# Optimization experiments

Measured on AMD Instinct MI355X. Metric: run time of the kernel, lower is better.

The kernel has to match this reference:

```python
import jax, jax.numpy as jnp
import numpy as np

HIDDEN = 2560
NH = 32            # num_attention_heads
HD = HIDDEN // NH  # head_size = 80
RD = 32            # rotary_dim = int(0.4 * 80)
THETA = 10000.0
B, S = 2, 2048


def _rope_cos_sin(position_ids):
    # neox-style partial RoPE over the first RD dims of each head
    inv_freq = 1.0 / (THETA ** (jnp.arange(0, RD, 2, dtype=jnp.float32) / RD))  # [RD/2]
    freqs = position_ids.astype(jnp.float32)[..., None] * inv_freq  # [B,S,RD/2]
    return jnp.cos(freqs), jnp.sin(freqs)


def _apply_rope(x, cos, sin):
    # x: [B,S,NH,HD]; rotate first RD dims (neox: halves are paired)
    rot, rest = x[..., :RD], x[..., RD:]
    x1, x2 = rot[..., : RD // 2], rot[..., RD // 2:]
    c = cos[:, :, None, :]
    s = sin[:, :, None, :]
    o1 = x1 * c - x2 * s
    o2 = x2 * c + x1 * s
    return jnp.concatenate([o1, o2, rest], axis=-1)


def setup_inputs() -> dict:
    key = jax.random.key(0)
    ks = jax.random.split(key, 6)
    position_ids = jnp.tile(jnp.arange(S, dtype=jnp.int64)[None, :], (B, 1))
    return {
        "position_ids": position_ids,
        "hidden_states": jax.random.normal(ks[0], (B, S, HIDDEN), dtype=jnp.float32),
        "w_qkv": jax.random.normal(ks[1], (HIDDEN, 3 * HIDDEN), dtype=jnp.float32) * 0.02,
        "b_qkv": jax.random.normal(ks[2], (3 * HIDDEN,), dtype=jnp.float32) * 0.02,
        "w_dense": jax.random.normal(ks[3], (HIDDEN, HIDDEN), dtype=jnp.float32) * 0.02,
        "b_dense": jax.random.normal(ks[4], (HIDDEN,), dtype=jnp.float32) * 0.02,
    }


def reference(position_ids, hidden_states, w_qkv, b_qkv, w_dense, b_dense):
    scale = HD ** -0.5
    qkv = hidden_states @ w_qkv + b_qkv          # [B,S,3*HIDDEN]
    q, k, v = jnp.split(qkv, 3, axis=-1)
    q = q.reshape(B, S, NH, HD)
    k = k.reshape(B, S, NH, HD)
    v = v.reshape(B, S, NH, HD)
    cos, sin = _rope_cos_sin(position_ids)
    q = _apply_rope(q, cos, sin)
    k = _apply_rope(k, cos, sin)
    scores = jnp.einsum("bqhd,bkhd->bhqk", q, k) * scale  # [B,NH,S,S]
    causal = jnp.tril(jnp.ones((S, S), dtype=bool))
    scores = jnp.where(causal[None, None], scores, jnp.finfo(scores.dtype).min)
    probs = jax.nn.softmax(scores, axis=-1)
    attn = jnp.einsum("bhqk,bkhd->bqhd", probs, v).reshape(B, S, HIDDEN)
    return attn @ w_dense + b_dense
```

## Files before the change

### kernel.cpp

```cpp
#include <hip/hip_runtime.h>

#define S_LEN 2048
#define NHEAD 32
#define HD 80
#define DPAD 96
#define HIDDEN 2560
#define QKV_N 7680

typedef __attribute__((ext_vector_type(8))) short bf16x8;
typedef __attribute__((ext_vector_type(8))) unsigned short u16x8;
typedef __attribute__((ext_vector_type(4))) float f32x4;

__device__ __forceinline__ unsigned short f2bf(float f) {
  unsigned int u = __float_as_uint(f);
  u += 0x7fffu + ((u >> 16) & 1u);
  return (unsigned short)(u >> 16);
}
__device__ __forceinline__ float bf2f(unsigned short h) {
  return __uint_as_float(((unsigned int)h) << 16);
}

__device__ __forceinline__ void gload16(const void* g, void* l) {
  __builtin_amdgcn_global_load_lds((const __attribute__((address_space(1))) void*)g,
                                   (__attribute__((address_space(3))) void*)l, 16, 0, 0);
}

__global__ __launch_bounds__(256) void k_cvt(const float* __restrict__ in,
                                             unsigned short* __restrict__ out, int n4) {
  int i = blockIdx.x * 256 + threadIdx.x;
  if (i >= n4) return;
  float4 v = reinterpret_cast<const float4*>(in)[i];
  ushort4 o;
  o.x = f2bf(v.x); o.y = f2bf(v.y); o.z = f2bf(v.z); o.w = f2bf(v.w);
  reinterpret_cast<ushort4*>(out)[i] = o;
}

__global__ __launch_bounds__(256) void k_transpose_bf16(const float* __restrict__ in,
                                                        unsigned short* __restrict__ out,
                                                        int R, int C) {
  __shared__ float tile[64][65];
  int tc = blockIdx.x * 64, tr = blockIdx.y * 64;
  for (int i = threadIdx.x; i < 64 * 64; i += 256) {
    int r = i >> 6, c = i & 63;
    tile[r][c] = in[(size_t)(tr + r) * C + (tc + c)];
  }
  __syncthreads();
  for (int i = threadIdx.x; i < 64 * 64; i += 256) {
    int r = i >> 6, c = i & 63;
    out[(size_t)(tc + r) * R + (tr + c)] = f2bf(tile[c][r]);
  }
}

__global__ __launch_bounds__(512, 2) void k_gemm256(const unsigned short* __restrict__ A,
                                                    const unsigned short* __restrict__ Bt,
                                                    const float* __restrict__ bias,
                                                    unsigned short* __restrict__ Cbf,
                                                    float* __restrict__ Cf,
                                                    int M, int N, int K, int out_f32) {
  __shared__ unsigned short sA[4][8192];
  __shared__ unsigned short sB[4][8192];
  const int nbn = N >> 8;
  const int nwg = (M >> 8) * nbn;
  int wg = blockIdx.x;
  const int cpx = nwg >> 3;
  wg = (wg & 7) * cpx + (wg >> 3);
  const int bm = wg / nbn, bn = wg - bm * nbn;
  const int tid = threadIdx.x;
  const int lane = tid & 63, wave = tid >> 6;
  const int wr = wave >> 2, wc = wave & 3;
  const int lc = lane & 15, lr = lane >> 4;

  const int sub = (lane & 7) ^ (lane >> 3);
  const int rstage = wave * 16 + (lane >> 3) * 2 + (sub >> 2);
  const int cstage = (sub & 3) * 8;
  const unsigned short* Agp = A + (size_t)(bm * 256 + rstage) * K + cstage;
  const unsigned short* Bgp = Bt + (size_t)(bn * 256 + rstage) * K + cstage;
  const size_t halfoff = (size_t)128 * K;

  const int laneoff = ((lc >> 1) << 7) + ((((lc & 1) << 2) | lr) ^ (lc >> 1)) << 4 ? 0 : 0;
  const int loff = ((lc >> 1) << 7) + (((((lc & 1) << 2) | lr) ^ (lc >> 1)) << 4);
  (void)laneoff;

  f32x4 acc[8][4];
  const f32x4 zero = {0.f, 0.f, 0.f, 0.f};
#pragma unroll
  for (int m = 0; m < 8; ++m)
#pragma unroll
    for (int n = 0; n < 4; ++n) acc[m][n] = zero;

  const int NT = K >> 5;

#pragma unroll
  for (int t = 0; t < 3; ++t) {
    gload16(Agp + 0 * halfoff + t * 32, &sA[t][wave * 512]);
    gload16(Agp + 1 * halfoff + t * 32, &sA[t][4096 + wave * 512]);
    gload16(Bgp + 0 * halfoff + t * 32, &sB[t][wave * 512]);
    gload16(Bgp + 1 * halfoff + t * 32, &sB[t][4096 + wave * 512]);
  }

  const char* cA[4] = {(const char*)&sA[0][0], (const char*)&sA[1][0],
                       (const char*)&sA[2][0], (const char*)&sA[3][0]};
  const char* cB[4] = {(const char*)&sB[0][0], (const char*)&sB[1][0],
                       (const char*)&sB[2][0], (const char*)&sB[3][0]};

  const int nj = NT >> 2;
  for (int j = 0; j < nj; ++j) {
#pragma unroll
    for (int to = 0; to < 4; ++to) {
      const int t = (j << 2) + to;
      if (t < NT - 2)       asm volatile("s_waitcnt vmcnt(8)" ::: "memory");
      else if (t == NT - 2) asm volatile("s_waitcnt vmcnt(4)" ::: "memory");
      else                  asm volatile("s_waitcnt vmcnt(0)" ::: "memory");
      __builtin_amdgcn_s_barrier();
      asm volatile("" ::: "memory");
      const bool st = (t + 3) < NT;
      const int sb = (to + 3) & 3;
      const char* bufA = cA[to];
      const char* bufB = cB[to];

      bf16x8 af[4], bfr[4];
#pragma unroll
      for (int mi = 0; mi < 4; ++mi)
        af[mi] = *(const bf16x8*)(bufA + ((wr * 128 + mi * 16) << 6) + loff);
#pragma unroll
      for (int ni = 0; ni < 4; ++ni)
        bfr[ni] = *(const bf16x8*)(bufB + ((wc * 64 + ni * 16) << 6) + loff);
      if (st) {
        gload16(Agp + 0 * halfoff + (t + 3) * 32, &sA[sb][wave * 512]);
        gload16(Agp + 1 * halfoff + (t + 3) * 32, &sA[sb][4096 + wave * 512]);
      }
      __builtin_amdgcn_s_barrier();
      asm volatile("s_waitcnt lgkmcnt(0)" ::: "memory");
      __builtin_amdgcn_sched_barrier(0);
      __builtin_amdgcn_s_setprio(1);
#pragma unroll
      for (int mi = 0; mi < 4; ++mi)
#pragma unroll
        for (int ni = 0; ni < 4; ++ni)
          acc[mi][ni] = __builtin_amdgcn_mfma_f32_16x16x32_bf16(af[mi], bfr[ni], acc[mi][ni], 0, 0, 0);
      __builtin_amdgcn_s_setprio(0);
      __builtin_amdgcn_s_barrier();

      bf16x8 ag[4];
#pragma unroll
      for (int mi = 0; mi < 4; ++mi)
        ag[mi] = *(const bf16x8*)(bufA + ((wr * 128 + (mi + 4) * 16) << 6) + loff);
      if (st) {
        gload16(Bgp + 0 * halfoff + (t + 3) * 32, &sB[sb][wave * 512]);
        gload16(Bgp + 1 * halfoff + (t + 3) * 32, &sB[sb][4096 + wave * 512]);
      }
      __builtin_amdgcn_s_barrier();
      asm volatile("s_waitcnt lgkmcnt(0)" ::: "memory");
      __builtin_amdgcn_sched_barrier(0);
      __builtin_amdgcn_s_setprio(1);
#pragma unroll
      for (int mi = 0; mi < 4; ++mi)
#pragma unroll
        for (int ni = 0; ni < 4; ++ni)
          acc[mi + 4][ni] = __builtin_amdgcn_mfma_f32_16x16x32_bf16(ag[mi], bfr[ni], acc[mi + 4][ni], 0, 0, 0);
      __builtin_amdgcn_s_setprio(0);
    }
  }

  const int rowb = bm * 256 + wr * 128;
  const int colb = bn * 256 + wc * 64;
#pragma unroll
  for (int ni = 0; ni < 4; ++ni) {
    const int col = colb + ni * 16 + lc;
    const float bv = bias[col];
#pragma unroll
    for (int mf = 0; mf < 8; ++mf) {
#pragma unroll
      for (int jj = 0; jj < 4; ++jj) {
        const int row = rowb + mf * 16 + lr * 4 + jj;
        const float v = acc[mf][ni][jj] + bv;
        if (out_f32) Cf[(size_t)row * N + col] = v;
        else Cbf[(size_t)row * N + col] = f2bf(v);
      }
    }
  }
}

__global__ __launch_bounds__(256) void k_rope(const unsigned short* __restrict__ qkv,
                                              unsigned short* __restrict__ Qw,
                                              unsigned short* __restrict__ Kw,
                                              unsigned short* __restrict__ Vt) {
  const int blk = blockIdx.x;
  const int sc = blk & 31;
  const int bh = blk >> 5;
  const int b = bh >> 5, h = bh & 31;
  const int s0 = sc * 64;
  __shared__ float cs0[64][16], sn0[64][16];
  __shared__ unsigned short vbuf[64][82];
  const int tid = threadIdx.x;
  for (int i = tid; i < 64 * 16; i += 256) {
    int sl = i >> 4, fi = i & 15;
    float ang = (float)(s0 + sl) * __expf(-(float)fi * 0.575646273248511421f);
    cs0[sl][fi] = cosf(ang);
    sn0[sl][fi] = sinf(ang);
  }
  __syncthreads();
  const size_t row0 = (size_t)(b * S_LEN + s0) * QKV_N;
  const size_t obase = ((size_t)bh * S_LEN + s0) * DPAD;
  for (int i = tid; i < 64 * DPAD; i += 256) {
    int sl = i / DPAD, d = i - sl * DPAD;
    float qv = 0.f, kv = 0.f;
    if (d < HD) {
      const unsigned short* rp = qkv + row0 + (size_t)sl * QKV_N + h * HD;
      float q = bf2f(rp[d]), k = bf2f(rp[HIDDEN + d]);
      if (d < 16) {
        float c = cs0[sl][d], s = sn0[sl][d];
        float q2 = bf2f(rp[d + 16]), k2 = bf2f(rp[HIDDEN + d + 16]);
        qv = q * c - q2 * s;
        kv = k * c - k2 * s;
      } else if (d < 32) {
        float c = cs0[sl][d - 16], s = sn0[sl][d - 16];
        float q1 = bf2f(rp[d - 16]), k1 = bf2f(rp[HIDDEN + d - 16]);
        qv = q * c + q1 * s;
        kv = k * c + k1 * s;
      } else {
        qv = q; kv = k;
      }
    }
    Qw[obase + (size_t)sl * DPAD + d] = f2bf(qv * 0.111803398874989485f);
    Kw[obase + (size_t)sl * DPAD + d] = f2bf(kv);
  }
  for (int i = tid; i < 64 * HD; i += 256) {
    int sl = i / HD, d = i - sl * HD;
    vbuf[sl][d] = qkv[row0 + (size_t)sl * QKV_N + 2 * HIDDEN + h * HD + d];
  }
  __syncthreads();
  const size_t vtb = (size_t)bh * DPAD * S_LEN + s0;
  for (int i = tid; i < DPAD * 64; i += 256) {
    int d = i >> 6, sl = i & 63;
    Vt[vtb + (size_t)d * S_LEN + sl] = (d < HD) ? vbuf[sl][d] : (unsigned short)0;
  }
}

__global__ __launch_bounds__(256, 2) void k_attn(const unsigned short* __restrict__ Qw,
                                                 const unsigned short* __restrict__ Kw,
                                                 const unsigned short* __restrict__ Vt,
                                                 unsigned short* __restrict__ O) {
  __shared__ unsigned short sK[2][64 * 104];
  __shared__ unsigned short sV[2][80 * 72];
  __shared__ unsigned short sP[4][16 * 72];
  const int p = blockIdx.x;
  const int bh = blockIdx.y;
  const int b = bh >> 5, h = bh & 31;
  const int tid = threadIdx.x;
  const int wave = tid >> 6, lane = tid & 63;
  const int lr = lane >> 4, lc = lane & 15;
  unsigned short* Pw = &sP[wave][0];

  const unsigned short* Kh = Kw + (size_t)bh * S_LEN * DPAD;
  const unsigned short* Vh = Vt + (size_t)bh * DPAD * S_LEN;
  const unsigned short* Qh = Qw + (size_t)bh * S_LEN * DPAD;

  const int kr = tid >> 2, kc = (tid & 3) * 24;
  const int vr = tid >> 3, vc = (tid & 7) * 8;

  u16x8 kst0, kst1, kst2, vst0, vst1, vst2;
  auto gload = [&](int t) {
    const unsigned short* Kg = Kh + ((size_t)(t * 64 + kr)) * DPAD + kc;
    kst0 = *(const u16x8*)(Kg);
    kst1 = *(const u16x8*)(Kg + 8);
    kst2 = *(const u16x8*)(Kg + 16);
    const unsigned short* Vg = Vh + (size_t)vr * S_LEN + t * 64 + vc;
    vst0 = *(const u16x8*)(Vg);
    vst1 = *(const u16x8*)(Vg + 32 * S_LEN);
    if (tid < 128) vst2 = *(const u16x8*)(Vg + (size_t)64 * S_LEN);
  };
  auto swrite = [&](int buf) {
    *(u16x8*)&sK[buf][kr * 104 + kc] = kst0;
    *(u16x8*)&sK[buf][kr * 104 + kc + 8] = kst1;
    *(u16x8*)&sK[buf][kr * 104 + kc + 16] = kst2;
    *(u16x8*)&sV[buf][vr * 72 + vc] = vst0;
    *(u16x8*)&sV[buf][(vr + 32) * 72 + vc] = vst1;
    if (tid < 128) *(u16x8*)&sV[buf][(vr + 64) * 72 + vc] = vst2;
  };

  const f32x4 zero = {0.f, 0.f, 0.f, 0.f};

#pragma unroll 1
  for (int qi = 0; qi < 2; ++qi) {
    const int qt = qi ? (15 - p) : p;
    const int nt = 2 * qt + 2;
    const int wbase = qt * 128 + wave * 32;

    bf16x8 qf[2][3];
#pragma unroll
    for (int m = 0; m < 2; ++m)
#pragma unroll
      for (int ks = 0; ks < 3; ++ks)
        qf[m][ks] = *(const bf16x8*)&Qh[(size_t)(wbase + m * 16 + lc) * DPAD + ks * 32 + lr * 8];

    f32x4 oacc[2][5];
#pragma unroll
    for (int m = 0; m < 2; ++m)
#pragma unroll
      for (int n = 0; n < 5; ++n) oacc[m][n] = zero;
    float mrun[2] = {-1e30f, -1e30f}, lrun[2] = {0.f, 0.f};

    gload(0);
    __syncthreads();
    swrite(0);
    int cur = 0;

#pragma unroll 1
    for (int t = 0; t < nt; ++t) {
      __syncthreads();
      if (t + 1 < nt) gload(t + 1);
      const int ktb = t * 64;
      const bool act0 = ktb <= wbase + 15;
      const bool act1 = ktb <= wbase + 31;
      if (act1) {
        const unsigned short* Kc = sK[cur];
        const unsigned short* Vc = sV[cur];
        f32x4 sf[2][4];
#pragma unroll
        for (int n = 0; n < 4; ++n) {
          sf[0][n] = zero; sf[1][n] = zero;
#pragma unroll
          for (int ks = 0; ks < 3; ++ks) {
            bf16x8 kf = *(const bf16x8*)&Kc[(n * 16 + lc) * 104 + ks * 32 + lr * 8];
            if (act0) sf[0][n] = __builtin_amdgcn_mfma_f32_16x16x32_bf16(kf, qf[0][ks], sf[0][n], 0, 0, 0);
            sf[1][n] = __builtin_amdgcn_mfma_f32_16x16x32_bf16(kf, qf[1][ks], sf[1][n], 0, 0, 0);
          }
        }
        bf16x8 vf[5][2];
#pragma unroll
        for (int n = 0; n < 5; ++n)
#pragma unroll
          for (int ks = 0; ks < 2; ++ks)
            vf[n][ks] = *(const bf16x8*)&Vc[(n * 16 + lc) * 72 + ks * 32 + lr * 8];
#pragma unroll
        for (int m = 0; m < 2; ++m) {
          if (m == 0 && !act0) continue;
          const int qrow0 = wbase + m * 16;
          if (ktb + 63 > qrow0) {
#pragma unroll
            for (int n = 0; n < 4; ++n)
#pragma unroll
              for (int j = 0; j < 4; ++j)
                if (ktb + n * 16 + lr * 4 + j > qrow0 + lc) sf[m][n][j] = -1e30f;
          }
          float t0 = sf[m][0][0];
#pragma unroll
          for (int n = 0; n < 4; ++n)
#pragma unroll
            for (int j = 0; j < 4; ++j) t0 = fmaxf(t0, sf[m][n][j]);
          t0 = fmaxf(t0, __shfl_xor(t0, 16));
          t0 = fmaxf(t0, __shfl_xor(t0, 32));
          const float nm = fmaxf(mrun[m], t0);
          const float corrq = __expf(mrun[m] - nm);
          mrun[m] = nm;
          float ps = 0.f;
#pragma unroll
          for (int n = 0; n < 4; ++n)
#pragma unroll
            for (int j = 0; j < 4; ++j) {
              float e = __expf(sf[m][n][j] - nm);
              sf[m][n][j] = e;
              ps += e;
            }
          ps += __shfl_xor(ps, 16);
          ps += __shfl_xor(ps, 32);
          lrun[m] = lrun[m] * corrq + ps;
          float cj[4];
#pragma unroll
          for (int j = 0; j < 4; ++j) cj[j] = __shfl(corrq, lr * 4 + j, 16);
#pragma unroll
          for (int n = 0; n < 5; ++n)
#pragma unroll
            for (int j = 0; j < 4; ++j) oacc[m][n][j] *= cj[j];
#pragma unroll
          for (int n = 0; n < 4; ++n) {
            unsigned lo = (unsigned)f2bf(sf[m][n][0]) | ((unsigned)f2bf(sf[m][n][1]) << 16);
            unsigned hi = (unsigned)f2bf(sf[m][n][2]) | ((unsigned)f2bf(sf[m][n][3]) << 16);
            uint2 u; u.x = lo; u.y = hi;
            *(uint2*)&Pw[lc * 72 + n * 16 + lr * 4] = u;
          }
          asm volatile("" ::: "memory");
          bf16x8 pa0 = *(const bf16x8*)&Pw[lc * 72 + lr * 8];
          bf16x8 pa1 = *(const bf16x8*)&Pw[lc * 72 + 32 + lr * 8];
#pragma unroll
          for (int n = 0; n < 5; ++n) {
            oacc[m][n] = __builtin_amdgcn_mfma_f32_16x16x32_bf16(pa0, vf[n][0], oacc[m][n], 0, 0, 0);
            oacc[m][n] = __builtin_amdgcn_mfma_f32_16x16x32_bf16(pa1, vf[n][1], oacc[m][n], 0, 0, 0);
          }
          asm volatile("" ::: "memory");
        }
      }
      if (t + 1 < nt) swrite(cur ^ 1);
      cur ^= 1;
    }

#pragma unroll
    for (int m = 0; m < 2; ++m) {
      float linv[4];
#pragma unroll
      for (int j = 0; j < 4; ++j) {
        float lj = __shfl(lrun[m], lr * 4 + j, 16);
        linv[j] = 1.f / lj;
      }
      const int q0 = wbase + m * 16 + lr * 4;
#pragma unroll
      for (int n = 0; n < 5; ++n) {
        const int d = n * 16 + lc;
#pragma unroll
        for (int j = 0; j < 4; ++j)
          O[((size_t)(b * S_LEN) + q0 + j) * HIDDEN + h * HD + d] = f2bf(oacc[m][n][j] * linv[j]);
      }
    }
  }
}

extern "C" void kernel_launch(void* const* d_in, const int* in_sizes, int n_in,
                              void* d_out, int out_size, void* d_ws, size_t ws_size,
                              hipStream_t stream) {
  (void)in_sizes; (void)n_in; (void)out_size; (void)ws_size;
  const float* hidden  = (const float*)d_in[1];
  const float* w_qkv   = (const float*)d_in[2];
  const float* b_qkv   = (const float*)d_in[3];
  const float* w_dense = (const float*)d_in[4];
  const float* b_dense = (const float*)d_in[5];
  char* ws = (char*)d_ws;
  unsigned short* Abf   = (unsigned short*)(ws + 0);
  unsigned short* Wqkvt = (unsigned short*)(ws + 20971520);
  unsigned short* Wdt   = (unsigned short*)(ws + 60293120);
  unsigned short* QKVb  = (unsigned short*)(ws + 73400320);
  unsigned short* Qw    = (unsigned short*)(ws + 136314880);
  unsigned short* Kw    = (unsigned short*)(ws + 161480704);
  unsigned short* Vt    = (unsigned short*)(ws + 186646528);
  unsigned short* Obf   = (unsigned short*)(ws + 211812352);

  k_cvt<<<10240, 256, 0, stream>>>(hidden, Abf, 2621440);
  k_transpose_bf16<<<dim3(120, 40), 256, 0, stream>>>(w_qkv, Wqkvt, 2560, 7680);
  k_transpose_bf16<<<dim3(40, 40), 256, 0, stream>>>(w_dense, Wdt, 2560, 2560);
  k_gemm256<<<480, 512, 0, stream>>>(Abf, Wqkvt, b_qkv, QKVb, nullptr, 4096, 7680, 2560, 0);
  k_rope<<<2048, 256, 0, stream>>>(QKVb, Qw, Kw, Vt);
  k_attn<<<dim3(8, 64), 256, 0, stream>>>(Qw, Kw, Vt, Obf);
  k_gemm256<<<160, 512, 0, stream>>>(Obf, Wdt, b_dense, nullptr, (float*)d_out, 4096, 2560, 2560, 1);
}
```

Baseline: 448.7 us.

## Split GEMM into QKV and output variants with smaller tiles for dense projection

```diff
diff --git a/kernel.cpp b/kernel.cpp
--- a/kernel.cpp
+++ b/kernel.cpp
@@ -51,12 +51,12 @@
   }
 }
 
-__global__ __launch_bounds__(512, 2) void k_gemm256(const unsigned short* __restrict__ A,
-                                                    const unsigned short* __restrict__ Bt,
-                                                    const float* __restrict__ bias,
-                                                    unsigned short* __restrict__ Cbf,
-                                                    float* __restrict__ Cf,
-                                                    int M, int N, int K, int out_f32) {
+__global__ __launch_bounds__(512, 2)
+void k_gemm_qkv(const unsigned short* __restrict__ A,
+                const unsigned short* __restrict__ Bt,
+                const float* __restrict__ bias,
+                unsigned short* __restrict__ Cbf,
+                int M, int N, int K) {
   __shared__ unsigned short sA[4][8192];
   __shared__ unsigned short sB[4][8192];
   const int nbn = N >> 8;
@@ -71,15 +71,13 @@
   const int lc = lane & 15, lr = lane >> 4;
 
   const int sub = (lane & 7) ^ (lane >> 3);
-  const int rstage = wave * 16 + (lane >> 3) * 2 + (sub >> 2);
+  const int rstage = wave * 16 + ((lane >> 3) << 1) + (sub >> 2);
   const int cstage = (sub & 3) * 8;
   const unsigned short* Agp = A + (size_t)(bm * 256 + rstage) * K + cstage;
   const unsigned short* Bgp = Bt + (size_t)(bn * 256 + rstage) * K + cstage;
   const size_t halfoff = (size_t)128 * K;
 
-  const int laneoff = ((lc >> 1) << 7) + ((((lc & 1) << 2) | lr) ^ (lc >> 1)) << 4 ? 0 : 0;
   const int loff = ((lc >> 1) << 7) + (((((lc & 1) << 2) | lr) ^ (lc >> 1)) << 4);
-  (void)laneoff;
 
   f32x4 acc[8][4];
   const f32x4 zero = {0.f, 0.f, 0.f, 0.f};
@@ -88,20 +86,16 @@
 #pragma unroll
     for (int n = 0; n < 4; ++n) acc[m][n] = zero;
 
+  auto stage = [&](int buf, int t) {
+    gload16(Agp + t * 32, &sA[buf][wave * 512]);
+    gload16(Agp + halfoff + t * 32, &sA[buf][4096 + wave * 512]);
+    gload16(Bgp + t * 32, &sB[buf][wave * 512]);
+    gload16(Bgp + halfoff + t * 32, &sB[buf][4096 + wave * 512]);
+  };
+
   const int NT = K >> 5;
-
-#pragma unroll
-  for (int t = 0; t < 3; ++t) {
-    gload16(Agp + 0 * halfoff + t * 32, &sA[t][wave * 512]);
-    gload16(Agp + 1 * halfoff + t * 32, &sA[t][4096 + wave * 512]);
-    gload16(Bgp + 0 * halfoff + t * 32, &sB[t][wave * 512]);
-    gload16(Bgp + 1 * halfoff + t * 32, &sB[t][4096 + wave * 512]);
-  }
-
-  const char* cA[4] = {(const char*)&sA[0][0], (const char*)&sA[1][0],
-                       (const char*)&sA[2][0], (const char*)&sA[3][0]};
-  const char* cB[4] = {(const char*)&sB[0][0], (const char*)&sB[1][0],
-                       (const char*)&sB[2][0], (const char*)&sB[3][0]};
+#pragma unroll
+  for (int t = 0; t < 3; ++t) stage(t, t);
 
   const int nj = NT >> 2;
   for (int j = 0; j < nj; ++j) {
@@ -113,52 +107,28 @@
       else                  asm volatile("s_waitcnt vmcnt(0)" ::: "memory");
       __builtin_amdgcn_s_barrier();
       asm volatile("" ::: "memory");
-      const bool st = (t + 3) < NT;
-      const int sb = (to + 3) & 3;
-      const char* bufA = cA[to];
-      const char* bufB = cB[to];
-
-      bf16x8 af[4], bfr[4];
-#pragma unroll
-      for (int mi = 0; mi < 4; ++mi)
+
+      const char* bufA = (const char*)&sA[to][0];
+      const char* bufB = (const char*)&sB[to][0];
+      bf16x8 af[8], bfr[4];
+#pragma unroll
+      for (int mi = 0; mi < 8; ++mi)
         af[mi] = *(const bf16x8*)(bufA + ((wr * 128 + mi * 16) << 6) + loff);
 #pragma unroll
       for (int ni = 0; ni < 4; ++ni)
         bfr[ni] = *(const bf16x8*)(bufB + ((wc * 64 + ni * 16) << 6) + loff);
-      if (st) {
-        gload16(Agp + 0 * halfoff + (t + 3) * 32, &sA[sb][wave * 512]);
-        gload16(Agp + 1 * halfoff + (t + 3) * 32, &sA[sb][4096 + wave * 512]);
-      }
-      __builtin_amdgcn_s_barrier();
+
+      if (t + 3 < NT) stage((to + 3) & 3, t + 3);
+
       asm volatile("s_waitcnt lgkmcnt(0)" ::: "memory");
       __builtin_amdgcn_sched_barrier(0);
       __builtin_amdgcn_s_setprio(1);
 #pragma unroll
-      for (int mi = 0; mi < 4; ++mi)
+      for (int mi = 0; mi < 8; ++mi)
 #pragma unroll
         for (int ni = 0; ni < 4; ++ni)
           acc[mi][ni] = __builtin_amdgcn_mfma_f32_16x16x32_bf16(af[mi], bfr[ni], acc[mi][ni], 0, 0, 0);
       __builtin_amdgcn_s_setprio(0);
-      __builtin_amdgcn_s_barrier();
-
-      bf16x8 ag[4];
-#pragma unroll
-      for (int mi = 0; mi < 4; ++mi)
-        ag[mi] = *(const bf16x8*)(bufA + ((wr * 128 + (mi + 4) * 16) << 6) + loff);
-      if (st) {
-        gload16(Bgp + 0 * halfoff + (t + 3) * 32, &sB[sb][wave * 512]);
-        gload16(Bgp + 1 * halfoff + (t + 3) * 32, &sB[sb][4096 + wave * 512]);
-      }
-      __builtin_amdgcn_s_barrier();
-      asm volatile("s_waitcnt lgkmcnt(0)" ::: "memory");
-      __builtin_amdgcn_sched_barrier(0);
-      __builtin_amdgcn_s_setprio(1);
-#pragma unroll
-      for (int mi = 0; mi < 4; ++mi)
-#pragma unroll
-        for (int ni = 0; ni < 4; ++ni)
-          acc[mi + 4][ni] = __builtin_amdgcn_mfma_f32_16x16x32_bf16(ag[mi], bfr[ni], acc[mi + 4][ni], 0, 0, 0);
-      __builtin_amdgcn_s_setprio(0);
     }
   }
 
@@ -173,9 +143,93 @@
 #pragma unroll
       for (int jj = 0; jj < 4; ++jj) {
         const int row = rowb + mf * 16 + lr * 4 + jj;
-        const float v = acc[mf][ni][jj] + bv;
-        if (out_f32) Cf[(size_t)row * N + col] = v;
-        else Cbf[(size_t)row * N + col] = f2bf(v);
+        Cbf[(size_t)row * N + col] = f2bf(acc[mf][ni][jj] + bv);
+      }
+    }
+  }
+}
+
+__global__ __launch_bounds__(256, 4)
+void k_gemm_out(const unsigned short* __restrict__ A,
+                const unsigned short* __restrict__ Bt,
+                const float* __restrict__ bias,
+                float* __restrict__ Cf,
+                int M, int N, int K) {
+  __shared__ unsigned short sA[2][4096];
+  __shared__ unsigned short sB[2][4096];
+  const int nbn = N >> 7;
+  const int nwg = (M >> 7) * nbn;
+  int wg = blockIdx.x;
+  const int cpx = nwg >> 3;
+  wg = (wg & 7) * cpx + (wg >> 3);
+  const int bm = wg / nbn, bn = wg - bm * nbn;
+  const int tid = threadIdx.x;
+  const int lane = tid & 63, wave = tid >> 6;
+  const int wr = wave >> 1, wc = wave & 1;
+  const int lc = lane & 15, lr = lane >> 4;
+
+  const int sub = (lane & 7) ^ (lane >> 3);
+  const int rstage = wave * 16 + ((lane >> 3) << 1) + (sub >> 2);
+  const int cstage = (sub & 3) * 8;
+  const unsigned short* Agp = A + (size_t)(bm * 128 + rstage) * K + cstage;
+  const unsigned short* Bgp = Bt + (size_t)(bn * 128 + rstage) * K + cstage;
+  const size_t halfoff = (size_t)64 * K;
+
+  const int loff = ((lc >> 1) << 7) + (((((lc & 1) << 2) | lr) ^ (lc >> 1)) << 4);
+
+  f32x4 acc[4][4];
+  const f32x4 zero = {0.f, 0.f, 0.f, 0.f};
+#pragma unroll
+  for (int m = 0; m < 4; ++m)
+#pragma unroll
+    for (int n = 0; n < 4; ++n) acc[m][n] = zero;
+
+  auto stage = [&](int buf, int t) {
+    gload16(Agp + t * 32, &sA[buf][wave * 512]);
+    gload16(Agp + halfoff + t * 32, &sA[buf][2048 + wave * 512]);
+    gload16(Bgp + t * 32, &sB[buf][wave * 512]);
+    gload16(Bgp + halfoff + t * 32, &sB[buf][2048 + wave * 512]);
+  };
+
+  const int NT = K >> 5;
+  stage(0, 0);
+  for (int t = 0; t < NT; ++t) {
+    asm volatile("s_waitcnt vmcnt(0)" ::: "memory");
+    __builtin_amdgcn_s_barrier();
+    asm volatile("" ::: "memory");
+    if (t + 1 < NT) stage((t + 1) & 1, t + 1);
+    const char* bufA = (const char*)&sA[t & 1][0];
+    const char* bufB = (const char*)&sB[t & 1][0];
+    bf16x8 af[4], bfr[4];
+#pragma unroll
+    for (int mi = 0; mi < 4; ++mi)
+      af[mi] = *(const bf16x8*)(bufA + ((wr * 64 + mi * 16) << 6) + loff);
+#pragma unroll
+    for (int ni = 0; ni < 4; ++ni)
+      bfr[ni] = *(const bf16x8*)(bufB + ((wc * 64 + ni * 16) << 6) + loff);
+    asm volatile("s_waitcnt lgkmcnt(0)" ::: "memory");
+    __builtin_amdgcn_sched_barrier(0);
+    __builtin_amdgcn_s_setprio(1);
+#pragma unroll
+    for (int mi = 0; mi < 4; ++mi)
+#pragma unroll
+      for (int ni = 0; ni < 4; ++ni)
+        acc[mi][ni] = __builtin_amdgcn_mfma_f32_16x16x32_bf16(af[mi], bfr[ni], acc[mi][ni], 0, 0, 0);
+    __builtin_amdgcn_s_setprio(0);
+  }
+
+  const int rowb = bm * 128 + wr * 64;
+  const int colb = bn * 128 + wc * 64;
+#pragma unroll
+  for (int ni = 0; ni < 4; ++ni) {
+    const int col = colb + ni * 16 + lc;
+    const float bv = bias[col];
+#pragma unroll
+    for (int mf = 0; mf < 4; ++mf) {
+#pragma unroll
+      for (int jj = 0; jj < 4; ++jj) {
+        const int row = rowb + mf * 16 + lr * 4 + jj;
+        Cf[(size_t)row * N + col] = acc[mf][ni][jj] + bv;
       }
     }
   }
@@ -437,8 +491,8 @@
   k_cvt<<<10240, 256, 0, stream>>>(hidden, Abf, 2621440);
   k_transpose_bf16<<<dim3(120, 40), 256, 0, stream>>>(w_qkv, Wqkvt, 2560, 7680);
   k_transpose_bf16<<<dim3(40, 40), 256, 0, stream>>>(w_dense, Wdt, 2560, 2560);
-  k_gemm256<<<480, 512, 0, stream>>>(Abf, Wqkvt, b_qkv, QKVb, nullptr, 4096, 7680, 2560, 0);
+  k_gemm_qkv<<<480, 512, 0, stream>>>(Abf, Wqkvt, b_qkv, QKVb, 4096, 7680, 2560);
   k_rope<<<2048, 256, 0, stream>>>(QKVb, Qw, Kw, Vt);
   k_attn<<<dim3(8, 64), 256, 0, stream>>>(Qw, Kw, Vt, Obf);
-  k_gemm256<<<160, 512, 0, stream>>>(Obf, Wdt, b_dense, nullptr, (float*)d_out, 4096, 2560, 2560, 1);
-}
+  k_gemm_out<<<640, 256, 0, stream>>>(Obf, Wdt, b_dense, (float*)d_out, 4096, 2560, 2560);
+}
```

Result: faster. 426.0 us (-5.0%).
